# Performance work log

Measured on AMD Instinct MI355X. Metric: run time of the kernel, lower is better.

## Reference

```python
import jax, jax.numpy as jnp
import numpy as np

VOXEL_SIZE = 0.4
GAMMA = 1.1  # VoxelPointsSampler.GAMMA
PC_MIN, PC_MAX = -75.2, 75.2


def setup_inputs() -> dict:
    key = jax.random.key(0)
    ks = jax.random.split(key, 6)
    N, M, C, S = 200000, 256, 5, 128
    xy = jax.random.uniform(ks[0], (N, 2), minval=PC_MIN, maxval=PC_MAX)
    z = jax.random.uniform(ks[1], (N, 1), minval=-2.0, maxval=4.0)
    feat = jax.random.normal(ks[2], (N, C - 3))
    points = jnp.concatenate([xy, z, feat], axis=1)  # [N, 5]
    ctr = jax.random.uniform(ks[3], (M, 2), minval=PC_MIN * 0.9, maxval=PC_MAX * 0.9)
    cz = jnp.zeros((M, 1), jnp.float32)
    dims = jax.random.uniform(ks[4], (M, 3), minval=1.0, maxval=5.0)
    yaw = jax.random.uniform(ks[5], (M, 1), minval=-3.14, maxval=3.14)
    boxes = jnp.concatenate([ctr, cz, dims, yaw], axis=1)  # [M, 7]
    pc_start = jnp.array([PC_MIN, PC_MIN], dtype=jnp.float32)
    return {"points": points, "boxes": boxes, "pc_start": pc_start, "num_sample": S}


def reference(points, boxes, pc_start, num_sample):
    N, C = points.shape
    M = boxes.shape[0]
    # --- voxel-level radius ball query (distances in voxel units) ---
    pcoords = (points[:, :2] - pc_start) / VOXEL_SIZE          # [N, 2]
    qcoords = (boxes[:, :2] - pc_start) / VOXEL_SIZE           # [M, 2]
    r_vox = jnp.linalg.norm(boxes[:, 3:5] * 0.5, axis=-1) * GAMMA / VOXEL_SIZE  # [M]
    dist = jnp.linalg.norm(qcoords[:, None, :] - pcoords[None, :, :], axis=-1)  # [M, N]
    vmask = (dist < r_vox[:, None]).any(axis=0)                # [N]
    # --- cylindrical pool (metric space); invalid points pushed out of every radius ---
    BIG = jnp.asarray(1e6, points.dtype)
    xy_m = jnp.where(vmask[:, None], points[:, :2], BIG)       # [N, 2]
    radii = jnp.linalg.norm(boxes[:, 3:5] * 0.5, axis=-1) * GAMMA  # [M]
    dis = jnp.linalg.norm(boxes[:, None, :2] - xy_m[None, :, :], axis=-1)  # [M, N]
    pmask = (dis <= radii[:, None]).astype(points.dtype)       # 0/1 [M, N]
    sm, sidx = jax.lax.top_k(pmask, num_sample)                # [M, S]
    smb = sm > 0.5                                             # bool [M, S]
    # unique indices across all sampled slots (fixed-size for jit)
    uniq, inv = jnp.unique(sidx.ravel(), return_inverse=True,
                           size=M * num_sample, fill_value=0)
    query_points = points[uniq]                                # [M*S, C] (padded)
    sampled_points = points[sidx] * smb[:, :, None]            # [M, S, C]
    idx = inv.reshape(M, num_sample).astype(jnp.int32) * smb   # [M, S]
    return sampled_points, idx, query_points
```

## Files before the change

### kernel.cpp

```cpp
#include <hip/hip_runtime.h>

typedef unsigned long long u64;
typedef unsigned short u16;
typedef unsigned char u8;

#define VOX 0.4f
#define GAM 1.1f
#define NCX 16
#define CELLW 32.0f
#define CAP 64

__device__ __forceinline__ float dist2d(float ax, float ay, float bx, float by) {
  float dx = __fsub_rn(ax, bx);
  float dy = __fsub_rn(ay, by);
  return __fsqrt_rn(__fadd_rn(__fmul_rn(dx, dx), __fmul_rn(dy, dy)));
}

__device__ __forceinline__ float box_radius(const float* __restrict__ boxes, int m) {
  float hx = __fmul_rn(boxes[m * 7 + 3], 0.5f);
  float hy = __fmul_rn(boxes[m * 7 + 4], 0.5f);
  float nr = __fsqrt_rn(__fadd_rn(__fmul_rn(hx, hx), __fmul_rn(hy, hy)));
  return __fmul_rn(nr, GAM);
}

__device__ __forceinline__ void box_voxel(const float* __restrict__ boxes, int m,
                                          float psx, float psy,
                                          float& qx, float& qy, float& r) {
  qx = __fdiv_rn(__fsub_rn(boxes[m * 7 + 0], psx), VOX);
  qy = __fdiv_rn(__fsub_rn(boxes[m * 7 + 1], psy), VOX);
  float hx = __fmul_rn(boxes[m * 7 + 3], 0.5f);
  float hy = __fmul_rn(boxes[m * 7 + 4], 0.5f);
  float nr = __fsqrt_rn(__fadd_rn(__fmul_rn(hx, hx), __fmul_rn(hy, hy)));
  r = __fdiv_rn(__fmul_rn(nr, GAM), VOX);
}

__global__ void k_prep(const float* __restrict__ boxes, const float* __restrict__ pc_start,
                       float* __restrict__ qxv, float* __restrict__ qyv, float* __restrict__ rv,
                       int* __restrict__ cellCnt, u16* __restrict__ cellList, int M) {
  const int tid = threadIdx.x;
  if (blockIdx.x == 0) {
    for (int m = tid; m < M; m += 256) {
      float qx, qy, r;
      box_voxel(boxes, m, pc_start[0], pc_start[1], qx, qy, r);
      qxv[m] = qx; qyv[m] = qy; rv[m] = r;
    }
    return;
  }
  const int cell = blockIdx.x - 1;
  const int cx = cell & (NCX - 1), cy = cell >> 4;
  const int wv = tid >> 6, lane = tid & 63;
  __shared__ int wcnt[4];
  const float x0 = (cx == 0) ? -3e38f : cx * CELLW;
  const float x1 = (cx == NCX - 1) ? 3e38f : (cx + 1) * CELLW;
  const float y0 = (cy == 0) ? -3e38f : cy * CELLW;
  const float y1 = (cy == NCX - 1) ? 3e38f : (cy + 1) * CELLW;
  bool hit = false;
  if (tid < M) {
    float qx, qy, r;
    box_voxel(boxes, tid, pc_start[0], pc_start[1], qx, qy, r);
    float ddx = fmaxf(0.0f, fmaxf(x0 - qx, qx - x1));
    float ddy = fmaxf(0.0f, fmaxf(y0 - qy, qy - y1));
    float rr = r + 0.01f;
    hit = (ddx * ddx + ddy * ddy <= rr * rr);
  }
  u64 b = __ballot(hit);
  if (lane == 0) wcnt[wv] = __popcll(b);
  __syncthreads();
  int base = 0;
  for (int w = 0; w < wv; ++w) base += wcnt[w];
  if (hit) {
    int slot = base + __popcll(b & ((1ULL << lane) - 1ULL));
    if (slot < CAP) cellList[cell * CAP + slot] = (u16)tid;
  }
  if (tid == 0) cellCnt[cell] = wcnt[0] + wcnt[1] + wcnt[2] + wcnt[3];
}

__global__ void k_vmask_count(const float* __restrict__ pts, const float* __restrict__ boxes,
                              const float* __restrict__ qxv, const float* __restrict__ qyv,
                              const float* __restrict__ rv,
                              const int* __restrict__ cellCnt, const u16* __restrict__ cellList,
                              u64* __restrict__ vbits, u8* __restrict__ present,
                              int* __restrict__ cnt, u64* __restrict__ bmG,
                              int* __restrict__ cpng,
                              const float* __restrict__ pc_start,
                              int N, int M, int nchunk) {
  __shared__ float cpx[256], cpy[256];
  __shared__ int cpn[256];
  __shared__ float sbx[256], sby[256], sbr[256];
  __shared__ u64 bm[256][4];
  __shared__ int wcnt[4];
  const int tid = threadIdx.x;
  const int blk = blockIdx.x;
  const int n = blk * 256 + tid;
  const int wv = tid >> 6, lane = tid & 63;
  const float psx = pc_start[0], psy = pc_start[1];
  const bool valid = (n < N);

  bm[tid][0] = 0; bm[tid][1] = 0; bm[tid][2] = 0; bm[tid][3] = 0;
  if (tid < M) {
    sbx[tid] = boxes[tid * 7 + 0];
    sby[tid] = boxes[tid * 7 + 1];
    sbr[tid] = box_radius(boxes, tid);
  }

  float px = 1e6f, py = 1e6f, pvx = 0.f, pvy = 0.f;
  if (valid) {
    px = pts[n * 5 + 0];
    py = pts[n * 5 + 1];
    pvx = __fdiv_rn(__fsub_rn(px, psx), VOX);
    pvy = __fdiv_rn(__fsub_rn(py, psy), VOX);
    present[n] = 0;
  }

  bool flag = false;
  if (valid) {
    int cx = (int)floorf(pvx * (1.0f / CELLW));
    int cy = (int)floorf(pvy * (1.0f / CELLW));
    cx = cx < 0 ? 0 : (cx > NCX - 1 ? NCX - 1 : cx);
    cy = cy < 0 ? 0 : (cy > NCX - 1 ? NCX - 1 : cy);
    const int cell = cy * NCX + cx;
    const int k = cellCnt[cell];
    if (k <= CAP) {
      for (int j = 0; j < k; ++j) {
        const int m = cellList[cell * CAP + j];
        float d = dist2d(qxv[m], qyv[m], pvx, pvy);
        if (d < rv[m]) { flag = true; break; }
      }
    } else {
      for (int m = 0; m < M; ++m) {
        float d = dist2d(qxv[m], qyv[m], pvx, pvy);
        if (d < rv[m]) { flag = true; break; }
      }
    }
  }
  u64 b = __ballot(flag);
  if (lane == 0) {
    vbits[n >> 6] = b;
    wcnt[wv] = __popcll(b);
  }
  __syncthreads();

  int base = 0;
  for (int w = 0; w < wv; ++w) base += wcnt[w];
  if (flag) {
    int slot = base + __popcll(b & ((1ULL << lane) - 1ULL));
    cpx[slot] = px;
    cpy[slot] = py;
    cpn[slot] = n;
  }
  __syncthreads();
  const int nfl = wcnt[0] + wcnt[1] + wcnt[2] + wcnt[3];
  if (tid < nfl) cpng[blk * 256 + tid] = cpn[tid];

  if (tid < nfl) {
    const float mx = cpx[tid], my = cpy[tid];
    float vx = __fdiv_rn(__fsub_rn(mx, psx), VOX);
    float vy = __fdiv_rn(__fsub_rn(my, psy), VOX);
    int cx = (int)floorf(vx * (1.0f / CELLW));
    int cy = (int)floorf(vy * (1.0f / CELLW));
    cx = cx < 0 ? 0 : (cx > NCX - 1 ? NCX - 1 : cx);
    cy = cy < 0 ? 0 : (cy > NCX - 1 ? NCX - 1 : cy);
    const int cell = cy * NCX + cx;
    const int k = cellCnt[cell];
    const u64 bit = 1ULL << (tid & 63);
    const int word = tid >> 6;
    if (k <= CAP) {
      for (int j = 0; j < k; ++j) {
        const int m = cellList[cell * CAP + j];
        float d = dist2d(sbx[m], sby[m], mx, my);
        if (d <= sbr[m]) atomicOr(&bm[m][word], bit);
      }
    } else {
      for (int m = 0; m < M; ++m) {
        float d = dist2d(sbx[m], sby[m], mx, my);
        if (d <= sbr[m]) atomicOr(&bm[m][word], bit);
      }
    }
  }
  __syncthreads();

  if (tid < M) {
    u64 w0 = bm[tid][0], w1 = bm[tid][1], w2 = bm[tid][2], w3 = bm[tid][3];
    u64* dst = bmG + ((size_t)blk * M + tid) * 4;
    dst[0] = w0; dst[1] = w1; dst[2] = w2; dst[3] = w3;
    cnt[tid * nchunk + blk] =
        __popcll(w0) + __popcll(w1) + __popcll(w2) + __popcll(w3);
  }
}

__global__ void __launch_bounds__(1024) k_scanbox(const int* __restrict__ cnt,
                                                  int* __restrict__ off,
                                                  int* __restrict__ kcount,
                                                  int nchunk, int M, int S) {
  __shared__ int s[1024];
  const int m = blockIdx.x, t = threadIdx.x;
  int v = (t < nchunk) ? cnt[m * nchunk + t] : 0;
  s[t] = v;
  __syncthreads();
  for (int d = 1; d < 1024; d <<= 1) {
    int x = (t >= d) ? s[t - d] : 0;
    __syncthreads();
    s[t] += x;
    __syncthreads();
  }
  if (t < nchunk) off[t * M + m] = s[t] - v;
  if (t == 1023) kcount[m] = (s[t] < S) ? s[t] : S;
}

__global__ void k_fillz(const float* __restrict__ pts, const float* __restrict__ boxes,
                        const u64* __restrict__ bmG, const int* __restrict__ cpng,
                        const int* __restrict__ off, const u64* __restrict__ vbits,
                        const int* __restrict__ kcount,
                        int* __restrict__ sidx, u8* __restrict__ present,
                        int N, int M, int S, int nchunk) {
  if ((int)blockIdx.x < nchunk) {
    const int c = blockIdx.x;
    const int m = threadIdx.x;
    if (m >= M) return;
    const u64* bp = bmG + ((size_t)c * M + m) * 4;
    u64 w0 = bp[0], w1 = bp[1], w2 = bp[2], w3 = bp[3];
    if (!(w0 | w1 | w2 | w3)) return;
    int cum = off[c * M + m];
    if (cum >= S) return;
    const int* pbase = cpng + c * 256;
    u64 ws[4] = {w0, w1, w2, w3};
    for (int wi = 0; wi < 4 && cum < S; ++wi) {
      u64 w = ws[wi];
      while (w && cum < S) {
        int j = (wi << 6) + __builtin_ctzll(w);
        w &= w - 1;
        int pn = pbase[j];
        sidx[m * S + cum] = pn;
        present[pn] = 1;
        ++cum;
      }
    }
  } else {
    const int m = blockIdx.x - nchunk;
    const int k0 = kcount[m];
    if (k0 >= S) return;
    const int lane = threadIdx.x;
    if (lane >= 64) return;
    const float bx = boxes[m * 7 + 0], by = boxes[m * 7 + 1];
    const float r = box_radius(boxes, m);
    const u64 ltmask = (1ULL << lane) - 1ULL;
    const int nwords = (N + 63) >> 6;
    int fill = k0;
    for (int wi = 0; wi < nwords && fill < S; ++wi) {
      const u64 w = vbits[wi];
      const int n = (wi << 6) + lane;
      bool one = false;
      if (n < N && ((w >> lane) & 1ULL)) {
        float d = dist2d(bx, by, pts[n * 5 + 0], pts[n * 5 + 1]);
        one = (d <= r);
      }
      const bool z = (n < N) && !one;
      u64 b = __ballot(z);
      if (z) {
        int pos = fill + __popcll(b & ltmask);
        if (pos < S) { sidx[m * S + pos] = n; present[n] = 1; }
      }
      fill += __popcll(b);
    }
  }
}

__global__ void k_bsum(const u8* __restrict__ present, int* __restrict__ bsum, int N) {
  const int n = blockIdx.x * 256 + threadIdx.x;
  bool f = (n < N) && present[n];
  u64 b = __ballot(f);
  __shared__ int ws[4];
  if ((threadIdx.x & 63) == 0) ws[threadIdx.x >> 6] = __popcll(b);
  __syncthreads();
  if (threadIdx.x == 0) bsum[blockIdx.x] = ws[0] + ws[1] + ws[2] + ws[3];
}

__global__ void __launch_bounds__(1024) k_scan(const int* __restrict__ bsum,
                                               int* __restrict__ boff, int nb) {
  __shared__ int s[1024];
  const int t = threadIdx.x;
  int v = (t < nb) ? bsum[t] : 0;
  s[t] = v;
  __syncthreads();
  for (int d = 1; d < 1024; d <<= 1) {
    int x = (t >= d) ? s[t - d] : 0;
    __syncthreads();
    s[t] += x;
    __syncthreads();
  }
  boff[t] = s[t] - v;
  if (t == nb - 1) boff[1024] = s[t];
}

__global__ void k_rank(const u8* __restrict__ present, const int* __restrict__ boff,
                       const float* __restrict__ pts, int* __restrict__ rank_arr,
                       float* __restrict__ out_query, int N) {
  const int t = threadIdx.x;
  const int n = blockIdx.x * 256 + t;
  bool f = (n < N) && present[n];
  u64 b = __ballot(f);
  __shared__ int ws[4];
  const int wv = t >> 6, lane = t & 63;
  if (lane == 0) ws[wv] = __popcll(b);
  __syncthreads();
  int base = boff[blockIdx.x];
  for (int w = 0; w < wv; ++w) base += ws[w];
  if (f) {
    int rank = base + __popcll(b & ((1ULL << lane) - 1ULL));
    rank_arr[n] = rank;
    float* q = out_query + (size_t)rank * 5;
    const float* p = pts + (size_t)n * 5;
    q[0] = p[0]; q[1] = p[1]; q[2] = p[2]; q[3] = p[3]; q[4] = p[4];
  }
}

__global__ void k_outpad(const float* __restrict__ pts, const int* __restrict__ sidx,
                         const int* __restrict__ kcount, const int* __restrict__ rank_arr,
                         const int* __restrict__ uptr,
                         float* __restrict__ out_samp, float* __restrict__ out_idx,
                         float* __restrict__ out_query, int MS, int S) {
  const int e = blockIdx.x * 256 + threadIdx.x;
  if (e >= MS) return;
  const int U = *uptr;
  if (e >= U) {
    float* q = out_query + (size_t)e * 5;
    q[0] = pts[0]; q[1] = pts[1]; q[2] = pts[2]; q[3] = pts[3]; q[4] = pts[4];
  }
  const int m = e / S;
  const int s = e - m * S;
  float* o = out_samp + (size_t)e * 5;
  if (s < kcount[m]) {
    int n = sidx[e];
    const float* p = pts + (size_t)n * 5;
    o[0] = p[0]; o[1] = p[1]; o[2] = p[2]; o[3] = p[3]; o[4] = p[4];
    out_idx[e] = (float)rank_arr[n];
  } else {
    o[0] = 0.f; o[1] = 0.f; o[2] = 0.f; o[3] = 0.f; o[4] = 0.f;
    out_idx[e] = 0.f;
  }
}

extern "C" void kernel_launch(void* const* d_in, const int* in_sizes, int n_in,
                              void* d_out, int out_size, void* d_ws, size_t ws_size,
                              hipStream_t stream) {
  const float* pts = (const float*)d_in[0];
  const float* boxes = (const float*)d_in[1];
  const float* pc_start = (const float*)d_in[2];
  const int N = in_sizes[0] / 5;
  const int M = in_sizes[1] / 7;
  const int S = out_size / (M * 11);
  const int MS = M * S;

  float* out_samp = (float*)d_out;
  float* out_idx = out_samp + (size_t)MS * 5;
  float* out_query = out_idx + (size_t)MS;

  const int nb = (N + 255) / 256;
  const int nchunk = nb;

  char* w = (char*)d_ws;
  auto take = [&](size_t bytes) {
    char* p = w;
    w += (bytes + 15) & ~(size_t)15;
    return (void*)p;
  };
  u64* vbits     = (u64*)take((size_t)(nb * 4) * 8);
  int* cnt       = (int*)take((size_t)M * nchunk * 4);
  int* off       = (int*)take((size_t)nchunk * M * 4);
  u64* bmG       = (u64*)take((size_t)nchunk * M * 4 * 8);
  int* cpng      = (int*)take((size_t)nchunk * 256 * 4);
  int* sidx      = (int*)take((size_t)MS * 4);
  int* kcount    = (int*)take((size_t)M * 4);
  int* rank_arr  = (int*)take((size_t)N * 4);
  int* bsum      = (int*)take((size_t)1024 * 4);
  int* boff      = (int*)take((size_t)1025 * 4);
  u8*  present   = (u8*)take((size_t)N);
  float* qxv     = (float*)take((size_t)M * 4);
  float* qyv     = (float*)take((size_t)M * 4);
  float* rv      = (float*)take((size_t)M * 4);
  int* cellCnt   = (int*)take((size_t)NCX * NCX * 4);
  u16* cellList  = (u16*)take((size_t)NCX * NCX * CAP * 2);

  k_prep<<<NCX * NCX + 1, 256, 0, stream>>>(boxes, pc_start, qxv, qyv, rv,
                                            cellCnt, cellList, M);
  k_vmask_count<<<nb, 256, 0, stream>>>(pts, boxes, qxv, qyv, rv, cellCnt, cellList,
                                        vbits, present, cnt, bmG, cpng,
                                        pc_start, N, M, nchunk);
  k_scanbox<<<M, 1024, 0, stream>>>(cnt, off, kcount, nchunk, M, S);
  k_fillz<<<nchunk + M, 256, 0, stream>>>(pts, boxes, bmG, cpng, off,
                                          vbits, kcount, sidx, present, N, M, S, nchunk);
  k_bsum<<<nb, 256, 0, stream>>>(present, bsum, N);
  k_scan<<<1, 1024, 0, stream>>>(bsum, boff, nb);
  k_rank<<<nb, 256, 0, stream>>>(present, boff, pts, rank_arr, out_query, N);
  k_outpad<<<(MS + 255) / 256, 256, 0, stream>>>(pts, sidx, kcount, rank_arr, boff + 1024,
                                                 out_samp, out_idx, out_query, MS, S);
}
```

Before: 95.56 us.

## Fuse per-box scan and fill into one kernel with wave-shuffle scan

Merges the per-box prefix scan over chunk counts and the sidx fill into a single kernel with one 1024-thread block per box. Popcounts are computed from the bitmaps in place of a separate count array, and the scan uses wave shuffles in place of a shared-memory Hillis-Steele loop. The zero-fill path now uses the whole block over 1024 points per step, where it previously used one wave. This removes a kernel launch and the cnt/off round trip through global memory. In exchange each box block reads strided bitmap entries and adds block barriers to the fill loop.

New measurement: 94.77 us. About the same (-0.8%).

```diff
diff --git a/kernel.cpp b/kernel.cpp
--- a/kernel.cpp
+++ b/kernel.cpp
@@ -80,10 +80,9 @@
                               const float* __restrict__ rv,
                               const int* __restrict__ cellCnt, const u16* __restrict__ cellList,
                               u64* __restrict__ vbits, u8* __restrict__ present,
-                              int* __restrict__ cnt, u64* __restrict__ bmG,
-                              int* __restrict__ cpng,
+                              u64* __restrict__ bmG, int* __restrict__ cpng,
                               const float* __restrict__ pc_start,
-                              int N, int M, int nchunk) {
+                              int N, int M) {
   __shared__ float cpx[256], cpy[256];
   __shared__ int cpn[256];
   __shared__ float sbx[256], sby[256], sbr[256];
@@ -180,52 +179,59 @@
   __syncthreads();
 
   if (tid < M) {
-    u64 w0 = bm[tid][0], w1 = bm[tid][1], w2 = bm[tid][2], w3 = bm[tid][3];
     u64* dst = bmG + ((size_t)blk * M + tid) * 4;
-    dst[0] = w0; dst[1] = w1; dst[2] = w2; dst[3] = w3;
-    cnt[tid * nchunk + blk] =
-        __popcll(w0) + __popcll(w1) + __popcll(w2) + __popcll(w3);
-  }
-}
-
-__global__ void __launch_bounds__(1024) k_scanbox(const int* __restrict__ cnt,
-                                                  int* __restrict__ off,
-                                                  int* __restrict__ kcount,
-                                                  int nchunk, int M, int S) {
-  __shared__ int s[1024];
-  const int m = blockIdx.x, t = threadIdx.x;
-  int v = (t < nchunk) ? cnt[m * nchunk + t] : 0;
-  s[t] = v;
-  __syncthreads();
-  for (int d = 1; d < 1024; d <<= 1) {
-    int x = (t >= d) ? s[t - d] : 0;
-    __syncthreads();
-    s[t] += x;
-    __syncthreads();
-  }
-  if (t < nchunk) off[t * M + m] = s[t] - v;
-  if (t == 1023) kcount[m] = (s[t] < S) ? s[t] : S;
-}
-
-__global__ void k_fillz(const float* __restrict__ pts, const float* __restrict__ boxes,
-                        const u64* __restrict__ bmG, const int* __restrict__ cpng,
-                        const int* __restrict__ off, const u64* __restrict__ vbits,
-                        const int* __restrict__ kcount,
-                        int* __restrict__ sidx, u8* __restrict__ present,
-                        int N, int M, int S, int nchunk) {
-  if ((int)blockIdx.x < nchunk) {
-    const int c = blockIdx.x;
-    const int m = threadIdx.x;
-    if (m >= M) return;
-    const u64* bp = bmG + ((size_t)c * M + m) * 4;
-    u64 w0 = bp[0], w1 = bp[1], w2 = bp[2], w3 = bp[3];
-    if (!(w0 | w1 | w2 | w3)) return;
-    int cum = off[c * M + m];
-    if (cum >= S) return;
-    const int* pbase = cpng + c * 256;
-    u64 ws[4] = {w0, w1, w2, w3};
+    dst[0] = bm[tid][0]; dst[1] = bm[tid][1];
+    dst[2] = bm[tid][2]; dst[3] = bm[tid][3];
+  }
+}
+
+__global__ void __launch_bounds__(1024) k_scanfill(
+    const float* __restrict__ pts, const float* __restrict__ boxes,
+    const u64* __restrict__ bmG, const int* __restrict__ cpng,
+    const u64* __restrict__ vbits, int* __restrict__ kcount,
+    int* __restrict__ sidx, u8* __restrict__ present,
+    int N, int M, int S, int nchunk) {
+  const int m = blockIdx.x;
+  const int t = threadIdx.x;
+  const int lane = t & 63, wv = t >> 6;
+  __shared__ int wsum[16];
+  __shared__ int zws[16];
+
+  u64 w0 = 0, w1 = 0, w2 = 0, w3 = 0;
+  int v = 0;
+  if (t < nchunk) {
+    const u64* bp = bmG + ((size_t)t * M + m) * 4;
+    w0 = bp[0]; w1 = bp[1]; w2 = bp[2]; w3 = bp[3];
+    v = __popcll(w0) + __popcll(w1) + __popcll(w2) + __popcll(w3);
+  }
+  int incl = v;
+  for (int d = 1; d < 64; d <<= 1) {
+    int x = __shfl_up(incl, d);
+    if (lane >= d) incl += x;
+  }
+  if (lane == 63) wsum[wv] = incl;
+  __syncthreads();
+  if (t < 16) {
+    int s = wsum[t];
+    for (int d = 1; d < 16; d <<= 1) {
+      int x = __shfl_up(s, d);
+      if (t >= d) s += x;
+    }
+    wsum[t] = s;
+  }
+  __syncthreads();
+  const int wbase = (wv > 0) ? wsum[wv - 1] : 0;
+  const int off = wbase + incl - v;
+  const int total = wsum[15];
+  const int k0 = total < S ? total : S;
+  if (t == 0) kcount[m] = k0;
+
+  if (t < nchunk && v > 0 && off < S) {
+    const int* pbase = cpng + t * 256;
+    int cum = off;
+    u64 ws4[4] = {w0, w1, w2, w3};
     for (int wi = 0; wi < 4 && cum < S; ++wi) {
-      u64 w = ws[wi];
+      u64 w = ws4[wi];
       while (w && cum < S) {
         int j = (wi << 6) + __builtin_ctzll(w);
         w &= w - 1;
@@ -235,33 +241,40 @@
         ++cum;
       }
     }
-  } else {
-    const int m = blockIdx.x - nchunk;
-    const int k0 = kcount[m];
-    if (k0 >= S) return;
-    const int lane = threadIdx.x;
-    if (lane >= 64) return;
-    const float bx = boxes[m * 7 + 0], by = boxes[m * 7 + 1];
-    const float r = box_radius(boxes, m);
-    const u64 ltmask = (1ULL << lane) - 1ULL;
-    const int nwords = (N + 63) >> 6;
-    int fill = k0;
-    for (int wi = 0; wi < nwords && fill < S; ++wi) {
-      const u64 w = vbits[wi];
-      const int n = (wi << 6) + lane;
-      bool one = false;
-      if (n < N && ((w >> lane) & 1ULL)) {
+  }
+
+  if (k0 >= S) return;
+  const float bx = boxes[m * 7 + 0], by = boxes[m * 7 + 1];
+  const float r = box_radius(boxes, m);
+  const u64 ltmask = (1ULL << lane) - 1ULL;
+  int fill = k0;
+  for (int p0 = 0; p0 < N && fill < S; p0 += 1024) {
+    const int n = p0 + t;
+    const bool validn = n < N;
+    bool one = false;
+    if (validn) {
+      u64 wbit = vbits[n >> 6];
+      if ((wbit >> (n & 63)) & 1ULL) {
         float d = dist2d(bx, by, pts[n * 5 + 0], pts[n * 5 + 1]);
         one = (d <= r);
       }
-      const bool z = (n < N) && !one;
-      u64 b = __ballot(z);
-      if (z) {
-        int pos = fill + __popcll(b & ltmask);
-        if (pos < S) { sidx[m * S + pos] = n; present[n] = 1; }
-      }
-      fill += __popcll(b);
-    }
+    }
+    const bool z = validn && !one;
+    u64 b = __ballot(z);
+    if (lane == 0) zws[wv] = __popcll(b);
+    __syncthreads();
+    int zbase = 0, ztot = 0;
+    for (int ww = 0; ww < 16; ++ww) {
+      int c = zws[ww];
+      if (ww < wv) zbase += c;
+      ztot += c;
+    }
+    if (z) {
+      int pos = fill + zbase + __popcll(b & ltmask);
+      if (pos < S) { sidx[m * S + pos] = n; present[n] = 1; }
+    }
+    fill += ztot;
+    __syncthreads();
   }
 }
 
@@ -365,8 +378,6 @@
     return (void*)p;
   };
   u64* vbits     = (u64*)take((size_t)(nb * 4) * 8);
-  int* cnt       = (int*)take((size_t)M * nchunk * 4);
-  int* off       = (int*)take((size_t)nchunk * M * 4);
   u64* bmG       = (u64*)take((size_t)nchunk * M * 4 * 8);
   int* cpng      = (int*)take((size_t)nchunk * 256 * 4);
   int* sidx      = (int*)take((size_t)MS * 4);
@@ -384,11 +395,9 @@
   k_prep<<<NCX * NCX + 1, 256, 0, stream>>>(boxes, pc_start, qxv, qyv, rv,
                                             cellCnt, cellList, M);
   k_vmask_count<<<nb, 256, 0, stream>>>(pts, boxes, qxv, qyv, rv, cellCnt, cellList,
-                                        vbits, present, cnt, bmG, cpng,
-                                        pc_start, N, M, nchunk);
-  k_scanbox<<<M, 1024, 0, stream>>>(cnt, off, kcount, nchunk, M, S);
-  k_fillz<<<nchunk + M, 256, 0, stream>>>(pts, boxes, bmG, cpng, off,
-                                          vbits, kcount, sidx, present, N, M, S, nchunk);
+                                        vbits, present, bmG, cpng, pc_start, N, M);
+  k_scanfill<<<M, 1024, 0, stream>>>(pts, boxes, bmG, cpng, vbits, kcount,
+                                     sidx, present, N, M, S, nchunk);
   k_bsum<<<nb, 256, 0, stream>>>(present, bsum, N);
   k_scan<<<1, 1024, 0, stream>>>(bsum, boff, nb);
   k_rank<<<nb, 256, 0, stream>>>(present, boff, pts, rank_arr, out_query, N);
```
